# Kernel tuning notes

Hardware: AMD Instinct MI355X
Metric: run time of the kernel (lower is better)

Reference implementation:

```python
import jax, jax.numpy as jnp
from jax import lax
import numpy as np

B, N, P, NB = 64, 16, 20, 30      # frames, boxes/frame, num_persons, num_behaviors
C, F, OUT, SR = 1024, 14, 3, 2    # fmap channels, fmap size, roi output, sampling ratio
EPS = 1e-5


def roi_align_one(fmap, boxes):
    """fmap: [C,H,W]; boxes: [K,4]=(x1,y1,x2,y2) in fmap coords. Returns [K,C,OUT,OUT].
    torchvision-style roi_align (aligned=False) with fixed sampling_ratio=SR."""
    H, W = fmap.shape[1], fmap.shape[2]
    x1, y1, x2, y2 = boxes[:, 0], boxes[:, 1], boxes[:, 2], boxes[:, 3]
    rw = jnp.maximum(x2 - x1, 1.0)
    rh = jnp.maximum(y2 - y1, 1.0)
    S = OUT * SR
    pos = (jnp.arange(S, dtype=fmap.dtype) + 0.5) / SR            # sample pos in bin units
    ys = jnp.clip(y1[:, None] + pos[None, :] * (rh / OUT)[:, None], 0.0, H - 1.0)  # [K,S]
    xs = jnp.clip(x1[:, None] + pos[None, :] * (rw / OUT)[:, None], 0.0, W - 1.0)
    y0 = jnp.floor(ys); x0 = jnp.floor(xs)
    y0i = y0.astype(jnp.int32); x0i = x0.astype(jnp.int32)
    y1i = jnp.minimum(y0i + 1, H - 1); x1i = jnp.minimum(x0i + 1, W - 1)
    wy = ys - y0; wx = xs - x0                                     # [K,S]
    g = lambda yi, xi: fmap[:, yi[:, :, None], xi[:, None, :]]     # [C,K,S,S]
    v = (g(y0i, x0i) * ((1 - wy)[:, :, None] * (1 - wx)[:, None, :])
         + g(y0i, x1i) * ((1 - wy)[:, :, None] * wx[:, None, :])
         + g(y1i, x0i) * (wy[:, :, None] * (1 - wx)[:, None, :])
         + g(y1i, x1i) * (wy[:, :, None] * wx[:, None, :]))
    v = jnp.transpose(v, (1, 0, 2, 3))                             # [K,C,S,S]
    K = boxes.shape[0]
    return v.reshape(K, C, OUT, SR, OUT, SR).mean(axis=(3, 5))     # avg over samples


roi_align = jax.vmap(roi_align_one, in_axes=(0, 0))


def bn(x, g, b, m, v):
    s = (g / jnp.sqrt(v + EPS))[None, :, None, None]
    return x * s + (b - m * g / jnp.sqrt(v + EPS))[None, :, None, None]


def leaky(x):
    return jnp.where(x > 0, x, 0.1 * x)


def behavior_conv(x, w1, g1, b1, m1, v1, w2, g2, b2, m2, v2):
    dn = ('NCHW', 'OIHW', 'NCHW')
    x = lax.conv_general_dilated(x, w1, (1, 1), 'SAME', dimension_numbers=dn)
    x = leaky(bn(x, g1, b1, m1, v1))
    x = lax.conv_general_dilated(x, w2, (1, 1), 'SAME', dimension_numbers=dn)
    return leaky(bn(x, g2, b2, m2, v2))


def forward(fmap, boxes, conv1_w, bn1_g, bn1_b, bn1_m, bn1_v,
            conv2_w, bn2_g, bn2_b, bn2_m, bn2_v,
            conv1d_w, conv1d_b, fc1_w, fc1_b, fc2_w, fc2_b, person_idx):
    # --- global feature: ROI over the whole fmap per frame ---
    gbox = jnp.broadcast_to(jnp.array([[0.0, 0.0, F, F]], jnp.float32), (B, 1, 4))
    g_roi = roi_align(fmap, gbox).reshape(B, C, OUT, OUT)          # [B,1024,3,3]
    g_feat = behavior_conv(g_roi, conv1_w, bn1_g, bn1_b, bn1_m, bn1_v,
                           conv2_w, bn2_g, bn2_b, bn2_m, bn2_v)    # [B,256,3,3]
    g_feat = g_feat.reshape(B, 256 * OUT * OUT)                    # [B,2304]

    # --- per-box ROI features ---
    i_roi = roi_align(fmap, boxes).reshape(B * N, C, OUT, OUT)     # [B*N,1024,3,3]
    i_feat = behavior_conv(i_roi, conv1_w, bn1_g, bn1_b, bn1_m, bn1_v,
                           conv2_w, bn2_g, bn2_b, bn2_m, bn2_v)
    i_feat = i_feat.reshape(B, N, 256 * OUT * OUT)                 # [B,N,2304]

    # --- scatter-accumulate into behavior tensor [B,P,2304] ---
    behavior = jnp.broadcast_to(g_feat[:, None, :], (B, P, 2304))
    bidx = jnp.broadcast_to(jnp.arange(B)[:, None], (B, N))
    behavior = behavior.at[bidx, person_idx].add(i_feat)

    # --- temporal conv1d across the batch axis for every person slot ---
    x = jnp.transpose(behavior, (1, 2, 0))                         # [P,2304,B]
    x = lax.conv_general_dilated(x, conv1d_w, (1,), 'SAME',
                                 dimension_numbers=('NCH', 'OIH', 'NCH'))
    x = x + conv1d_b[None, :, None]                                # [P,2304,B]

    # --- gather each (frame, box)'s person feature at its frame and classify ---
    x = jnp.transpose(x, (2, 0, 1))                                # [B,P,2304]
    feats = jnp.take_along_axis(x, person_idx[:, :, None], axis=1) # [B,N,2304]
    h = jax.nn.relu(feats @ fc1_w + fc1_b)                         # dropout off (eval)
    return h @ fc2_w + fc2_b                                       # [B,N,NB]


def setup_inputs() -> dict:
    key = jax.random.key(0)
    ks = jax.random.split(key, 16)
    fmap = jax.random.normal(ks[0], (B, C, F, F), jnp.float32)
    lo = jax.random.uniform(ks[1], (B, N, 2), jnp.float32, 0.0, 9.0)
    sz = jax.random.uniform(ks[2], (B, N, 2), jnp.float32, 2.0, 5.0)
    hi = jnp.minimum(lo + sz, float(F))
    boxes = jnp.concatenate([lo, hi], axis=-1)                     # (x1,y1,x2,y2)
    person_idx = jax.random.randint(ks[3], (B, N), 0, P)
    s = lambda k, shape, fan: jax.random.normal(k, shape, jnp.float32) / np.sqrt(fan)
    return {
        'fmap': fmap, 'boxes': boxes, 'person_idx': person_idx,
        'conv1_w': s(ks[4], (512, 1024, 3, 3), 1024 * 9),
        'bn1_g': jnp.ones(512), 'bn1_b': jnp.zeros(512),
        'bn1_m': jnp.zeros(512), 'bn1_v': jnp.ones(512),
        'conv2_w': s(ks[5], (256, 512, 3, 3), 512 * 9),
        'bn2_g': jnp.ones(256), 'bn2_b': jnp.zeros(256),
        'bn2_m': jnp.zeros(256), 'bn2_v': jnp.ones(256),
        'conv1d_w': s(ks[6], (2304, 2304, 3), 2304 * 3),
        'conv1d_b': jnp.zeros(2304),
        'fc1_w': s(ks[7], (2304, 1024), 2304), 'fc1_b': jnp.zeros(1024),
        'fc2_w': s(ks[8], (1024, NB), 1024), 'fc2_b': jnp.zeros(NB),
    }


def reference(fmap, boxes, person_idx, conv1_w, bn1_g, bn1_b, bn1_m, bn1_v,
              conv2_w, bn2_g, bn2_b, bn2_m, bn2_v,
              conv1d_w, conv1d_b, fc1_w, fc1_b, fc2_w, fc2_b):
    return forward(fmap, boxes, conv1_w, bn1_g, bn1_b, bn1_m, bn1_v,
                   conv2_w, bn2_g, bn2_b, bn2_m, bn2_v,
                   conv1d_w, conv1d_b, fc1_w, fc1_b, fc2_w, fc2_b, person_idx)
```

## Files before the change

### kernel.cpp

```cpp
#include <hip/hip_runtime.h>
#include <hip/hip_bf16.h>
#include <cstdint>
#include <cstddef>

typedef __bf16 bf16;
typedef __bf16 bf16x8 __attribute__((ext_vector_type(8)));
typedef float f32x4 __attribute__((ext_vector_type(4)));

__device__ __forceinline__ void gload_lds16(const bf16* g, bf16* l) {
    __builtin_amdgcn_global_load_lds((const __attribute__((address_space(1))) void*)g,
                                     (__attribute__((address_space(3))) void*)l, 16, 0, 0);
}

__device__ __forceinline__ int block_tap_mask(int y) {
    int lo = (y * 128) / 1088;
    int hiRow = y * 128 + 127; if (hiRow > 9791) hiRow = 9791;
    int hi = hiRow / 1088;
    int msk = 0;
    for (int pos = lo; pos <= hi; ++pos) {
        int oy = pos / 3, ox = pos - oy * 3;
        int ym = oy == 0 ? 6 : (oy == 1 ? 7 : 3);
        int xm = ox == 0 ? 6 : (ox == 1 ? 7 : 3);
        #pragma unroll
        for (int ty = 0; ty < 3; ty++)
            #pragma unroll
            for (int tx = 0; tx < 3; tx++)
                if (((ym >> ty) & 1) & ((xm >> tx) & 1))
                    msk |= 1 << (ty * 3 + tx);
    }
    return msk;
}

template <int NT>
__global__ void __launch_bounds__(256) repack_w(const float* __restrict__ w, bf16* __restrict__ out,
                                                int OC, int IC) {
    int idx = blockIdx.x * 256 + threadIdx.x;
    if (idx >= OC * IC) return;
    int oc = idx / IC;
    int ic = idx - oc * IC;
    const float* src = w + (size_t)idx * NT;
    #pragma unroll
    for (int t = 0; t < NT; t++)
        out[(size_t)oc * NT * IC + t * IC + ic] = (bf16)src[t];
}

__global__ void __launch_bounds__(256) transpose_fc1(const float* __restrict__ w, bf16* __restrict__ out) {
    __shared__ float t[32][33];
    int iT = blockIdx.x * 32;
    int oT = blockIdx.y * 32;
    int tx = threadIdx.x, ty = threadIdx.y;
    #pragma unroll
    for (int j = 0; j < 4; j++)
        t[ty + j * 8][tx] = w[(size_t)(iT + ty + j * 8) * 1024 + oT + tx];
    __syncthreads();
    #pragma unroll
    for (int j = 0; j < 4; j++)
        out[(size_t)(oT + ty + j * 8) * 2304 + iT + tx] = (bf16)t[tx][ty + j * 8];
}

__global__ void __launch_bounds__(256) setup_all(int* __restrict__ rb1t, int* __restrict__ rb2t,
                                                 int* __restrict__ rb1dg, int* __restrict__ rbid,
                                                 int* __restrict__ tapmask,
                                                 int* __restrict__ tasks1, int* __restrict__ tasks2,
                                                 const int* __restrict__ pidx,
                                                 bf16* __restrict__ zp1, bf16* __restrict__ zp2,
                                                 bf16* __restrict__ zp3,
                                                 const float* g1, const float* b1, const float* m1, const float* v1,
                                                 const float* g2, const float* b2, const float* m2, const float* v2,
                                                 float* __restrict__ s1, float* __restrict__ t1,
                                                 float* __restrict__ s2, float* __restrict__ t2,
                                                 const float* __restrict__ fc2_w, bf16* __restrict__ w2t) {
    int m = blockIdx.x * 256 + threadIdx.x;
    if (m < 9 * 9856) {
        int tap = m / 9856, r = m - tap * 9856;
        int mm = r < 9792 ? r : 0;
        int pos = mm / 1088, img = mm - pos * 1088;
        int oy = pos / 3, ox = pos - oy * 3;
        int ty = tap / 3, tx = tap - ty * 3;
        int iy = oy + ty - 1, ix = ox + tx - 1;
        bool valid = (iy >= 0) & (iy < 3) & (ix >= 0) & (ix < 3);
        int cell = iy * 3 + ix;
        rb1t[m] = valid ? 1024 + (img * 9 + cell) * 1024 : 0;
        rb2t[m] = valid ? 512 + (cell * 1088 + img) * 512 : 0;
    }
    if (m < 77) tapmask[m] = block_tap_mask(m);
    if (blockIdx.x == 0) {
        __shared__ int sJ[77], sBase[78];
        __shared__ int ey[164], ej[164], ew[164];
        int t = threadIdx.x;
        if (t < 77) sJ[t] = (__popc(block_tap_mask(t)) + 2) / 3;
        __syncthreads();
        if (t == 0) {
            int acc = 0;
            for (int y = 0; y < 77; ++y) { sBase[y] = acc; acc += sJ[y]; }
            sBase[77] = acc;
        }
        __syncthreads();
        if (t < 77) {
            int T = __popc(block_tap_mask(t));
            int J = sJ[t];
            int w[3] = {0, 0, 0};
            for (int o = 0; o < T; ++o) w[o * J / T]++;
            for (int jj = 0; jj < J; ++jj) {
                int e = sBase[t] + jj;
                ey[e] = t; ej[e] = jj; ew[e] = w[jj];
            }
        }
        __syncthreads();
        if (t < 164) {
            int wv = ew[t], rank = 0;
            for (int e2 = 0; e2 < 164; ++e2)
                rank += (ew[e2] > wv) | ((ew[e2] == wv) & (e2 < t));
            int pk = (ey[t] << 5) | (ej[t] << 2);
            #pragma unroll
            for (int nt = 0; nt < 4; ++nt) tasks1[rank * 4 + nt] = pk | nt;
            #pragma unroll
            for (int nt = 0; nt < 2; ++nt) tasks2[rank * 2 + nt] = pk | nt;
        }
    }
    if (m < 3 * 1024) {
        int tap = m / 1024, r = m - tap * 1024;
        int b = r >> 4;
        int p = pidx[r];
        int tt = b + tap - 1;
        bool valid = (tt >= 0) & (tt < 64);
        rb1dg[m] = valid ? 2304 + (p * 64 + tt) * 2304 : 0;
    }
    if (m < 1024) rbid[m] = m * 2304;
    if (m < 30 * 1024) {
        int n = m / 1024, k = m - n * 1024;
        w2t[m] = (bf16)fc2_w[(size_t)k * 30 + n];
    }
    if (m < 1024) zp1[m] = (bf16)0.f;
    if (m < 512)  zp2[m] = (bf16)0.f;
    if (m < 2304) zp3[m] = (bf16)0.f;
    if (m < 512) {
        float sc = g1[m] * rsqrtf(v1[m] + 1e-5f);
        s1[m] = sc; t1[m] = b1[m] - m1[m] * sc;
    } else if (m < 768) {
        int i = m - 512;
        float sc = g2[i] * rsqrtf(v2[i] + 1e-5f);
        s2[i] = sc; t2[i] = b2[i] - m2[i] * sc;
    }
}

__global__ void __launch_bounds__(256) transpose_fmap(const float* __restrict__ fmap, bf16* __restrict__ fml) {
    __shared__ float t[32][33];
    int img = blockIdx.z;
    int hwT = blockIdx.x * 32;
    int cT  = blockIdx.y * 32;
    int tx = threadIdx.x, ty = threadIdx.y;
    #pragma unroll
    for (int j = 0; j < 4; j++) {
        int c = cT + ty + j * 8;
        int hw = hwT + tx;
        if (hw < 196)
            t[ty + j * 8][tx] = fmap[((size_t)img * 1024 + c) * 196 + hw];
    }
    __syncthreads();
    #pragma unroll
    for (int j = 0; j < 4; j++) {
        int hw = hwT + ty + j * 8;
        int c = cT + tx;
        if (hw < 196)
            fml[((size_t)img * 196 + hw) * 1024 + c] = (bf16)t[tx][ty + j * 8];
    }
}

__global__ void __launch_bounds__(128) roi_kernel2(const bf16* __restrict__ fml, const float* __restrict__ boxes,
                                                   bf16* __restrict__ a1c) {
    int box = blockIdx.x;
    int tid = threadIdx.x;
    float x1, y1, x2, y2;
    int img;
    if (box < 64) { img = box; x1 = 0.f; y1 = 0.f; x2 = 14.f; y2 = 14.f; }
    else {
        int ib = box - 64;
        img = ib >> 4;
        const float* bb = boxes + (size_t)ib * 4;
        x1 = bb[0]; y1 = bb[1]; x2 = bb[2]; y2 = bb[3];
    }
    float rw = fmaxf(x2 - x1, 1.f), rh = fmaxf(y2 - y1, 1.f);
    __shared__ float swy[6], swx[6];
    __shared__ int sy0[6], sx0[6];
    if (tid < 6) {
        int i = tid;
        float pos = ((float)i + 0.5f) * 0.5f;
        float yv = fminf(fmaxf(y1 + pos * (rh * (1.f / 3.f)), 0.f), 13.f);
        float y0 = floorf(yv);
        sy0[i] = (int)y0; swy[i] = yv - y0;
        float xv = fminf(fmaxf(x1 + pos * (rw * (1.f / 3.f)), 0.f), 13.f);
        float x0 = floorf(xv);
        sx0[i] = (int)x0; swx[i] = xv - x0;
    }
    __syncthreads();
    const bf16* base = fml + (size_t)img * 196 * 1024 + tid * 8;
    #pragma unroll
    for (int oy = 0; oy < 3; oy++) {
        #pragma unroll
        for (int ox = 0; ox < 3; ox++) {
            float acc[8];
            #pragma unroll
            for (int e = 0; e < 8; e++) acc[e] = 0.f;
            #pragma unroll
            for (int dy = 0; dy < 2; dy++) {
                int sy = 2 * oy + dy;
                int y0 = sy0[sy]; float wy = swy[sy];
                int y1i = min(y0 + 1, 13);
                #pragma unroll
                for (int dx = 0; dx < 2; dx++) {
                    int sx = 2 * ox + dx;
                    int x0 = sx0[sx]; float wx = swx[sx];
                    int x1i = min(x0 + 1, 13);
                    bf16x8 f00 = *(const bf16x8*)(base + (size_t)(y0 * 14 + x0) * 1024);
                    bf16x8 f01 = *(const bf16x8*)(base + (size_t)(y0 * 14 + x1i) * 1024);
                    bf16x8 f10 = *(const bf16x8*)(base + (size_t)(y1i * 14 + x0) * 1024);
                    bf16x8 f11 = *(const bf16x8*)(base + (size_t)(y1i * 14 + x1i) * 1024);
                    float w00 = (1.f - wy) * (1.f - wx), w01 = (1.f - wy) * wx;
                    float w10 = wy * (1.f - wx),         w11 = wy * wx;
                    #pragma unroll
                    for (int e = 0; e < 8; e++)
                        acc[e] += w00 * (float)f00[e] + w01 * (float)f01[e]
                                + w10 * (float)f10[e] + w11 * (float)f11[e];
                }
            }
            bf16x8 o;
            #pragma unroll
            for (int e = 0; e < 8; e++) o[e] = (bf16)(acc[e] * 0.25f);
            *(bf16x8*)(a1c + 1024 + ((size_t)box * 9 + oy * 3 + ox) * 1024 + tid * 8) = o;
        }
    }
}

__global__ void __launch_bounds__(256) assemble(const float* __restrict__ feat, const int* __restrict__ pidx,
                                                bf16* __restrict__ asm3) {
    int b = blockIdx.x;
    int p = blockIdx.y;
    __shared__ int idxs[16];
    if (threadIdx.x < 16) idxs[threadIdx.x] = pidx[b * 16 + threadIdx.x];
    __syncthreads();
    const float* g = feat + (size_t)b * 2304;
    for (int f = threadIdx.x; f < 2304; f += 256) {
        float v = g[f];
        #pragma unroll
        for (int n = 0; n < 16; n++)
            if (idxs[n] == p) v += feat[(size_t)(64 + b * 16 + n) * 2304 + f];
        asm3[2304 + ((size_t)p * 64 + b) * 2304 + f] = (bf16)v;
    }
}

template <int MODE, int NSPLIT>
__global__ void __launch_bounds__(256) gemm_k(const bf16* __restrict__ A, const int* __restrict__ rowtab,
                                              const bf16* __restrict__ Bw, float* __restrict__ outp,
                                              const int* __restrict__ tapmask,
                                              const int* __restrict__ tasklist) {
    constexpr int K   = MODE == 0 ? 9216 : MODE == 1 ? 4608 : MODE == 2 ? 6912 : 2304;
    constexpr int N   = MODE == 0 ? 512  : MODE == 1 ? 256  : MODE == 2 ? 2304 : 1024;
    constexpr int Cin = MODE == 0 ? 1024 : MODE == 1 ? 512  : 2304;
    constexpr int M   = MODE <= 1 ? 9792 : 1024;
    constexpr int MT  = MODE <= 1 ? 9856 : 1024;
    constexpr bool MPAD = (M % 128) != 0;
    constexpr int KTS = (K / 64) / NSPLIT;

    const int tid = threadIdx.x;
    const int lane = tid & 63, wave = tid >> 6;
    const int q = lane >> 4, ln16 = lane & 15;
    const int wr = wave >> 1, wc = wave & 1;

    __shared__ __align__(16) bf16 As[128 * 64];
    __shared__ __align__(16) bf16 Bs[128 * 64];

    const int sr = lane >> 3;
    const int sc = ((lane & 7) ^ sr) * 8;

    int bm, bn, z;
    int mask = 0, T = 0, J = 0, jsel = 0;
    if constexpr (MODE <= 1) {
        const int pk = tasklist[blockIdx.x];
        const int y = pk >> 5;
        jsel = (pk >> 2) & 7;
        const int nt = pk & 3;
        bm = y * 128; bn = nt * 128; z = jsel;
        mask = tapmask[y];
        T = __popc(mask);
        J = (T + 2) / 3;
    } else {
        bm = blockIdx.y * 128;
        bn = blockIdx.x * 128;
        z = blockIdx.z;
    }

    const bf16* gB[4];
    #pragma unroll
    for (int u = 0; u < 4; u++)
        gB[u] = Bw + (size_t)(bn + wave * 32 + u * 8 + sr) * K + sc;

    f32x4 acc[4][4];
    #pragma unroll
    for (int mt = 0; mt < 4; mt++)
        #pragma unroll
        for (int nn = 0; nn < 4; nn++)
            acc[mt][nn] = (f32x4){0.f, 0.f, 0.f, 0.f};

    if constexpr (MODE <= 1) {
        int ord = 0;
        for (int tap = 0; tap < 9; ++tap) {
            if (!((mask >> tap) & 1)) continue;
            const int o = ord++;
            if (o * J / T != jsel) continue;
            int rbA[4];
            #pragma unroll
            for (int u = 0; u < 4; u++)
                rbA[u] = rowtab[tap * MT + bm + wave * 32 + u * 8 + sr];
            for (int kk = 0; kk < Cin / 64; ++kk) {
                const int aoff = kk * 64 + sc;
                const int k0 = tap * Cin + kk * 64;

                __syncthreads();
                #pragma unroll
                for (int u = 0; u < 4; u++)
                    gload_lds16(A + (size_t)(rbA[u] + aoff), As + (wave * 32 + u * 8) * 64);
                #pragma unroll
                for (int u = 0; u < 4; u++)
                    gload_lds16(gB[u] + k0, Bs + (wave * 32 + u * 8) * 64);
                __syncthreads();

                #pragma unroll
                for (int s = 0; s < 2; s++) {
                    bf16x8 af[4], bfr[4];
                    #pragma unroll
                    for (int mt = 0; mt < 4; mt++) {
                        int r = wr * 64 + mt * 16 + ln16;
                        af[mt] = *(const bf16x8*)(As + r * 64 + (((4 * s + q) ^ (ln16 & 7)) << 3));
                    }
                    #pragma unroll
                    for (int nn = 0; nn < 4; nn++) {
                        int r = wc * 64 + nn * 16 + ln16;
                        bfr[nn] = *(const bf16x8*)(Bs + r * 64 + (((4 * s + q) ^ (ln16 & 7)) << 3));
                    }
                    #pragma unroll
                    for (int mt = 0; mt < 4; mt++)
                        #pragma unroll
                        for (int nn = 0; nn < 4; nn++)
                            acc[mt][nn] = __builtin_amdgcn_mfma_f32_16x16x32_bf16(af[mt], bfr[nn], acc[mt][nn], 0, 0, 0);
                }
            }
        }
    } else {
        int rbA[4];
        int curtap = -1;
        for (int kt = z * KTS; kt < z * KTS + KTS; kt++) {
            const int k0 = kt * 64;
            const int tap = k0 / Cin;
            const int inner = k0 - tap * Cin;
            if (tap != curtap) {
                curtap = tap;
                #pragma unroll
                for (int u = 0; u < 4; u++)
                    rbA[u] = rowtab[tap * MT + bm + wave * 32 + u * 8 + sr];
            }
            const int aoff = inner + sc;

            __syncthreads();
            #pragma unroll
            for (int u = 0; u < 4; u++)
                gload_lds16(A + (size_t)(rbA[u] + aoff), As + (wave * 32 + u * 8) * 64);
            #pragma unroll
            for (int u = 0; u < 4; u++)
                gload_lds16(gB[u] + k0, Bs + (wave * 32 + u * 8) * 64);
            __syncthreads();

            #pragma unroll
            for (int s = 0; s < 2; s++) {
                bf16x8 af[4], bfr[4];
                #pragma unroll
                for (int mt = 0; mt < 4; mt++) {
                    int r = wr * 64 + mt * 16 + ln16;
                    af[mt] = *(const bf16x8*)(As + r * 64 + (((4 * s + q) ^ (ln16 & 7)) << 3));
                }
                #pragma unroll
                for (int nn = 0; nn < 4; nn++) {
                    int r = wc * 64 + nn * 16 + ln16;
                    bfr[nn] = *(const bf16x8*)(Bs + r * 64 + (((4 * s + q) ^ (ln16 & 7)) << 3));
                }
                #pragma unroll
                for (int mt = 0; mt < 4; mt++)
                    #pragma unroll
                    for (int nn = 0; nn < 4; nn++)
                        acc[mt][nn] = __builtin_amdgcn_mfma_f32_16x16x32_bf16(af[mt], bfr[nn], acc[mt][nn], 0, 0, 0);
            }
        }
    }

    #pragma unroll
    for (int mt = 0; mt < 4; mt++) {
        int gmBase = bm + wr * 64 + mt * 16 + q * 4;
        #pragma unroll
        for (int r = 0; r < 4; r++) {
            int gm = gmBase + r;
            if (MPAD && gm >= M) continue;
            #pragma unroll
            for (int nn = 0; nn < 4; nn++) {
                int gn = bn + wc * 64 + nn * 16 + ln16;
                outp[((size_t)z * M + gm) * N + gn] = acc[mt][nn][r];
            }
        }
    }
}

__global__ void __launch_bounds__(256) reduce0_tiled(const float* __restrict__ part,
                                                     float* __restrict__ feat,
                                                     const float* __restrict__ s2, const float* __restrict__ t2,
                                                     const int* __restrict__ tapm) {
    int c = blockIdx.x;
    int t = threadIdx.x;
    float acc[9];
    #pragma unroll
    for (int r = 0; r < 9; r++) {
        int m = r * 1088 + c;
        int y = m >> 7;
        int J = (__popc(tapm[y]) + 2) / 3;
        const float* p0 = part + (size_t)m * 256 + t;
        float v = p0[0] + p0[(size_t)9792 * 256];
        if (J == 3) v += p0[(size_t)2 * 9792 * 256];
        acc[r] = v;
    }
    float s = s2[t], b = t2[t];
    __shared__ float L[9 * 257];
    #pragma unroll
    for (int r = 0; r < 9; r++) {
        float v = acc[r] * s + b;
        v = v > 0.f ? v : 0.1f * v;
        L[r * 257 + t] = v;
    }
    __syncthreads();
    float* fout = feat + (size_t)c * 2304;
    #pragma unroll
    for (int k = 0; k < 9; k++) {
        int f = t + k * 256;
        int oc = f / 9, pos = f - oc * 9;
        fout[f] = L[pos * 257 + oc];
    }
}

template <int RMODE>
__global__ void __launch_bounds__(256) reduce_k(const float* __restrict__ part, void* __restrict__ outp,
                                                const float* __restrict__ c0, const float* __restrict__ c1,
                                                const int* __restrict__ tapm) {
    constexpr int M = RMODE == 1 ? 1024 : RMODE == 2 ? 1024 : 9792;
    constexpr int N = RMODE == 1 ? 2304 : RMODE == 2 ? 1024 : 512;
    constexpr int S = RMODE == 1 ? 4    : RMODE == 2 ? 6    : 2;
    int idx = blockIdx.x * 256 + threadIdx.x;
    if (idx >= M * N) return;
    int m = idx / N, n = idx - m * N;
    float v = 0.f;
    #pragma unroll
    for (int s = 0; s < S; s++) v += part[(size_t)s * M * N + idx];
    if constexpr (RMODE == 1) {
        v += c0[n];
        ((bf16*)outp)[idx] = (bf16)v;
    } else if constexpr (RMODE == 2) {
        v = fmaxf(v + c0[n], 0.f);
        ((bf16*)outp)[idx] = (bf16)v;
    } else {
        int y = m >> 7;
        int J = (__popc(tapm[y]) + 2) / 3;
        if (J == 3) v += part[(size_t)2 * M * N + idx];
        v = v * c0[n] + c1[n];
        v = v > 0.f ? v : 0.1f * v;
        ((bf16*)outp)[512 + (size_t)m * 512 + n] = (bf16)v;
    }
}

__global__ void __launch_bounds__(256) fc2_kernel(const bf16* __restrict__ h, const bf16* __restrict__ w2t,
                                                  const float* __restrict__ b2, float* __restrict__ out) {
    int tid = threadIdx.x;
    int m = blockIdx.x * 8 + (tid >> 5);
    int n = tid & 31;
    int n2 = n < 30 ? n : 29;
    const bf16* hr = h + (size_t)m * 1024;
    const bf16* wr = w2t + (size_t)n2 * 1024;
    float acc = 0.f;
    for (int k = 0; k < 1024; k += 8) {
        bf16x8 hv = *(const bf16x8*)(hr + k);
        bf16x8 wv = *(const bf16x8*)(wr + k);
        #pragma unroll
        for (int e = 0; e < 8; e++) acc += (float)hv[e] * (float)wv[e];
    }
    if (n < 30) out[(size_t)m * 30 + n] = acc + b2[n];
}

extern "C" void kernel_launch(void* const* d_in, const int* in_sizes, int n_in,
                              void* d_out, int out_size, void* d_ws, size_t ws_size,
                              hipStream_t stream) {
    const float* fmap     = (const float*)d_in[0];
    const float* boxes    = (const float*)d_in[1];
    const int*   pidx     = (const int*)d_in[2];
    const float* conv1_w  = (const float*)d_in[3];
    const float* bn1_g    = (const float*)d_in[4];
    const float* bn1_b    = (const float*)d_in[5];
    const float* bn1_m    = (const float*)d_in[6];
    const float* bn1_v    = (const float*)d_in[7];
    const float* conv2_w  = (const float*)d_in[8];
    const float* bn2_g    = (const float*)d_in[9];
    const float* bn2_b    = (const float*)d_in[10];
    const float* bn2_m    = (const float*)d_in[11];
    const float* bn2_v    = (const float*)d_in[12];
    const float* conv1d_w = (const float*)d_in[13];
    const float* conv1d_b = (const float*)d_in[14];
    const float* fc1_w    = (const float*)d_in[15];
    const float* fc1_b    = (const float*)d_in[16];
    const float* fc2_w    = (const float*)d_in[17];
    const float* fc2_b    = (const float*)d_in[18];
    float* out = (float*)d_out;

    char* ws = (char*)d_ws;

    float* s1    = (float*)(ws + 0);
    float* t1    = (float*)(ws + 2048);
    float* s2    = (float*)(ws + 4096);
    float* t2    = (float*)(ws + 5120);
    int*   rbid  = (int*)(ws + 6144);
    int*   rb1dg = (int*)(ws + 10240);
    int*   tapm  = (int*)(ws + 22528);
    int*   rb1t  = (int*)(ws + 25600);
    int*   rb2t  = (int*)(ws + 380416);
    int*   tasks1 = (int*)(ws + 735232);
    int*   tasks2 = (int*)(ws + 738944);
    bf16*  fml    = (bf16*)(ws + 768000);
    float* part1  = (float*)(ws + 768000);
    float* part2  = (float*)(ws + 768000);
    float* part1d = (float*)(ws + 768000);
    float* partfc = (float*)(ws + 768000);
    bf16*  a1c    = (bf16*)(ws + 60930048);
    bf16*  wb1d   = (bf16*)(ws + 60930048);
    bf16*  fc1t   = (bf16*)(ws + 92780544);
    bf16*  xbuf   = (bf16*)(ws + 97499136);
    bf16*  hbuf   = (bf16*)(ws + 102217728);
    bf16*  w2t    = (bf16*)(ws + 104314880);
    bf16*  wb1    = (bf16*)(ws + 104857600);
    bf16*  wb2    = (bf16*)(ws + 114294784);
    bf16*  a2c    = (bf16*)(ws + 116654080);
    bf16*  asm3   = (bf16*)(ws + 126682112);
    float* feat   = (float*)(ws + 132584960);

    bf16* zp1 = a1c;
    bf16* zp2 = a2c;
    bf16* zp3 = asm3;

    setup_all<<<(9 * 9856 + 255) / 256, 256, 0, stream>>>(rb1t, rb2t, rb1dg, rbid, tapm,
                                                          tasks1, tasks2, pidx,
                                                          zp1, zp2, zp3,
                                                          bn1_g, bn1_b, bn1_m, bn1_v,
                                                          bn2_g, bn2_b, bn2_m, bn2_v,
                                                          s1, t1, s2, t2, fc2_w, w2t);
    repack_w<9><<<(512 * 1024 + 255) / 256, 256, 0, stream>>>(conv1_w, wb1, 512, 1024);
    repack_w<9><<<(256 * 512 + 255) / 256, 256, 0, stream>>>(conv2_w, wb2, 256, 512);

    transpose_fmap<<<dim3(7, 32, 64), dim3(32, 8), 0, stream>>>(fmap, fml);
    roi_kernel2<<<1088, 128, 0, stream>>>(fml, boxes, a1c);

    gemm_k<0, 3><<<656, 256, 0, stream>>>(a1c, rb1t, wb1, part1, tapm, tasks1);
    reduce_k<3><<<(9792 * 512 + 255) / 256, 256, 0, stream>>>(part1, a2c, s1, t1, tapm);

    repack_w<3><<<(2304 * 2304 + 255) / 256, 256, 0, stream>>>(conv1d_w, wb1d, 2304, 2304);
    transpose_fc1<<<dim3(72, 32), dim3(32, 8), 0, stream>>>(fc1_w, fc1t);

    gemm_k<1, 3><<<328, 256, 0, stream>>>(a2c, rb2t, wb2, part2, tapm, tasks2);
    reduce0_tiled<<<1088, 256, 0, stream>>>(part2, feat, s2, t2, tapm);
    assemble<<<dim3(64, 20), 256, 0, stream>>>(feat, pidx, asm3);
    gemm_k<2, 4><<<dim3(18, 8, 4), 256, 0, stream>>>(asm3, rb1dg, wb1d, part1d, tapm, nullptr);
    reduce_k<1><<<(1024 * 2304 + 255) / 256, 256, 0, stream>>>(part1d, xbuf, conv1d_b, nullptr, nullptr);
    gemm_k<3, 6><<<dim3(8, 8, 6), 256, 0, stream>>>(xbuf, rbid, fc1t, partfc, tapm, nullptr);
    reduce_k<2><<<(1024 * 1024 + 255) / 256, 256, 0, stream>>>(partfc, hbuf, fc1_b, nullptr, nullptr);
    fc2_kernel<<<128, 256, 0, stream>>>(hbuf, w2t, fc2_b, out);
    (void)in_sizes; (void)n_in; (void)out_size; (void)ws_size;
}
```

Before: 456.5 us.

## Retune split-K factors, reorder task lists per XCD, fuse conv weight repacks

Lowers the split-K factor for the conv2 task GEMM (taps split into groups of up to four), the conv1d GEMM and the fc1 GEMM, cutting partial-sum traffic and reduction work. The setup kernel builds separate task lists for conv1 and conv2 and interleaves task indices in groups of eight, likely to spread heavy tasks across chiplets. The two 3x3 weight repack kernels merge into one launch. Fewer splits mean fewer blocks and longer per-block K loops, which may reduce occupancy.

New measurement: 465.0 us. About the same (+1.9%).

```diff
diff --git a/kernel.cpp b/kernel.cpp
--- a/kernel.cpp
+++ b/kernel.cpp
@@ -42,6 +42,27 @@
     #pragma unroll
     for (int t = 0; t < NT; t++)
         out[(size_t)oc * NT * IC + t * IC + ic] = (bf16)src[t];
+}
+
+__global__ void __launch_bounds__(256) repack_w9_both(const float* __restrict__ wa, bf16* __restrict__ oa,
+                                                      const float* __restrict__ wb, bf16* __restrict__ ob) {
+    int idx = blockIdx.x * 256 + threadIdx.x;
+    if (idx < 512 * 1024) {
+        int oc = idx >> 10, ic = idx & 1023;
+        const float* src = wa + (size_t)idx * 9;
+        #pragma unroll
+        for (int t = 0; t < 9; t++)
+            oa[(size_t)oc * 9216 + t * 1024 + ic] = (bf16)src[t];
+    } else {
+        int k = idx - 512 * 1024;
+        if (k < 256 * 512) {
+            int oc = k >> 9, ic = k & 511;
+            const float* src = wb + (size_t)k * 9;
+            #pragma unroll
+            for (int t = 0; t < 9; t++)
+                ob[(size_t)oc * 4608 + t * 512 + ic] = (bf16)src[t];
+        }
+    }
 }
 
 __global__ void __launch_bounds__(256) transpose_fc1(const float* __restrict__ w, bf16* __restrict__ out) {
@@ -85,37 +106,60 @@
     }
     if (m < 77) tapmask[m] = block_tap_mask(m);
     if (blockIdx.x == 0) {
-        __shared__ int sJ[77], sBase[78];
-        __shared__ int ey[164], ej[164], ew[164];
+        __shared__ int sT[77], sB1[78], sB2[78];
+        __shared__ int e1y[164], e1j[164], e1w[164];
+        __shared__ int e2y[130], e2j[130], e2w[130];
         int t = threadIdx.x;
-        if (t < 77) sJ[t] = (__popc(block_tap_mask(t)) + 2) / 3;
+        if (t < 77) sT[t] = __popc(block_tap_mask(t));
         __syncthreads();
         if (t == 0) {
-            int acc = 0;
-            for (int y = 0; y < 77; ++y) { sBase[y] = acc; acc += sJ[y]; }
-            sBase[77] = acc;
+            int a1 = 0, a2 = 0;
+            for (int y = 0; y < 77; ++y) {
+                sB1[y] = a1; a1 += (sT[y] + 2) / 3;
+                sB2[y] = a2; a2 += (sT[y] + 3) / 4;
+            }
+            sB1[77] = a1;
+            sB2[77] = a2;
         }
         __syncthreads();
         if (t < 77) {
-            int T = __popc(block_tap_mask(t));
-            int J = sJ[t];
-            int w[3] = {0, 0, 0};
-            for (int o = 0; o < T; ++o) w[o * J / T]++;
-            for (int jj = 0; jj < J; ++jj) {
-                int e = sBase[t] + jj;
-                ey[e] = t; ej[e] = jj; ew[e] = w[jj];
+            int T = sT[t];
+            int J1 = (T + 2) / 3, J2 = (T + 3) / 4;
+            int w1[3] = {0, 0, 0}, w2[3] = {0, 0, 0};
+            for (int o = 0; o < T; ++o) { w1[o * J1 / T]++; w2[o * J2 / T]++; }
+            for (int jj = 0; jj < J1; ++jj) {
+                int e = sB1[t] + jj;
+                e1y[e] = t; e1j[e] = jj; e1w[e] = w1[jj];
+            }
+            for (int jj = 0; jj < J2; ++jj) {
+                int e = sB2[t] + jj;
+                e2y[e] = t; e2j[e] = jj; e2w[e] = w2[jj];
             }
         }
         __syncthreads();
         if (t < 164) {
-            int wv = ew[t], rank = 0;
-            for (int e2 = 0; e2 < 164; ++e2)
-                rank += (ew[e2] > wv) | ((ew[e2] == wv) & (e2 < t));
-            int pk = (ey[t] << 5) | (ej[t] << 2);
-            #pragma unroll
-            for (int nt = 0; nt < 4; ++nt) tasks1[rank * 4 + nt] = pk | nt;
-            #pragma unroll
-            for (int nt = 0; nt < 2; ++nt) tasks2[rank * 2 + nt] = pk | nt;
+            int wv = e1w[t], rank = 0;
+            for (int e2i = 0; e2i < 164; ++e2i)
+                rank += (e1w[e2i] > wv) | ((e1w[e2i] == wv) & (e2i < t));
+            int pk = (e1y[t] << 5) | (e1j[t] << 2);
+            #pragma unroll
+            for (int nt = 0; nt < 4; ++nt) {
+                int idx = (rank < 160) ? ((rank & 7) + (((rank >> 3) * 4 + nt) << 3))
+                                       : (640 + (rank - 160) * 4 + nt);
+                tasks1[idx] = pk | nt;
+            }
+        }
+        if (t < 130) {
+            int wv = e2w[t], rank = 0;
+            for (int e2i = 0; e2i < 130; ++e2i)
+                rank += (e2w[e2i] > wv) | ((e2w[e2i] == wv) & (e2i < t));
+            int pk = (e2y[t] << 5) | (e2j[t] << 2);
+            #pragma unroll
+            for (int nt = 0; nt < 2; ++nt) {
+                int idx = (rank < 128) ? ((rank & 7) + (((rank >> 3) * 2 + nt) << 3))
+                                       : (256 + (rank - 128) * 2 + nt);
+                tasks2[idx] = pk | nt;
+            }
         }
     }
     if (m < 3 * 1024) {
@@ -283,7 +327,7 @@
         bm = y * 128; bn = nt * 128; z = jsel;
         mask = tapmask[y];
         T = __popc(mask);
-        J = (T + 2) / 3;
+        J = MODE == 0 ? (T + 2) / 3 : (T + 3) / 4;
     } else {
         bm = blockIdx.y * 128;
         bn = blockIdx.x * 128;
@@ -419,10 +463,11 @@
     for (int r = 0; r < 9; r++) {
         int m = r * 1088 + c;
         int y = m >> 7;
-        int J = (__popc(tapm[y]) + 2) / 3;
+        int J = (__popc(tapm[y]) + 3) / 4;
         const float* p0 = part + (size_t)m * 256 + t;
-        float v = p0[0] + p0[(size_t)9792 * 256];
-        if (J == 3) v += p0[(size_t)2 * 9792 * 256];
+        float v = p0[0];
+        if (J >= 2) v += p0[(size_t)9792 * 256];
+        if (J >= 3) v += p0[(size_t)2 * 9792 * 256];
         acc[r] = v;
     }
     float s = s2[t], b = t2[t];
@@ -449,7 +494,7 @@
                                                 const int* __restrict__ tapm) {
     constexpr int M = RMODE == 1 ? 1024 : RMODE == 2 ? 1024 : 9792;
     constexpr int N = RMODE == 1 ? 2304 : RMODE == 2 ? 1024 : 512;
-    constexpr int S = RMODE == 1 ? 4    : RMODE == 2 ? 6    : 2;
+    constexpr int S = RMODE == 1 ? 3    : RMODE == 2 ? 4    : 2;
     int idx = blockIdx.x * 256 + threadIdx.x;
     if (idx >= M * N) return;
     int m = idx / N, n = idx - m * N;
@@ -554,8 +599,7 @@
                                                           bn1_g, bn1_b, bn1_m, bn1_v,
                                                           bn2_g, bn2_b, bn2_m, bn2_v,
                                                           s1, t1, s2, t2, fc2_w, w2t);
-    repack_w<9><<<(512 * 1024 + 255) / 256, 256, 0, stream>>>(conv1_w, wb1, 512, 1024);
-    repack_w<9><<<(256 * 512 + 255) / 256, 256, 0, stream>>>(conv2_w, wb2, 256, 512);
+    repack_w9_both<<<2560, 256, 0, stream>>>(conv1_w, wb1, conv2_w, wb2);
 
     transpose_fmap<<<dim3(7, 32, 64), dim3(32, 8), 0, stream>>>(fmap, fml);
     roi_kernel2<<<1088, 128, 0, stream>>>(fml, boxes, a1c);
@@ -566,12 +610,12 @@
     repack_w<3><<<(2304 * 2304 + 255) / 256, 256, 0, stream>>>(conv1d_w, wb1d, 2304, 2304);
     transpose_fc1<<<dim3(72, 32), dim3(32, 8), 0, stream>>>(fc1_w, fc1t);
 
-    gemm_k<1, 3><<<328, 256, 0, stream>>>(a2c, rb2t, wb2, part2, tapm, tasks2);
+    gemm_k<1, 3><<<260, 256, 0, stream>>>(a2c, rb2t, wb2, part2, tapm, tasks2);
     reduce0_tiled<<<1088, 256, 0, stream>>>(part2, feat, s2, t2, tapm);
     assemble<<<dim3(64, 20), 256, 0, stream>>>(feat, pidx, asm3);
-    gemm_k<2, 4><<<dim3(18, 8, 4), 256, 0, stream>>>(asm3, rb1dg, wb1d, part1d, tapm, nullptr);
+    gemm_k<2, 3><<<dim3(18, 8, 3), 256, 0, stream>>>(asm3, rb1dg, wb1d, part1d, tapm, nullptr);
     reduce_k<1><<<(1024 * 2304 + 255) / 256, 256, 0, stream>>>(part1d, xbuf, conv1d_b, nullptr, nullptr);
-    gemm_k<3, 6><<<dim3(8, 8, 6), 256, 0, stream>>>(xbuf, rbid, fc1t, partfc, tapm, nullptr);
+    gemm_k<3, 4><<<dim3(8, 8, 4), 256, 0, stream>>>(xbuf, rbid, fc1t, partfc, tapm, nullptr);
     reduce_k<2><<<(1024 * 1024 + 255) / 256, 256, 0, stream>>>(partfc, hbuf, fc1_b, nullptr, nullptr);
     fc2_kernel<<<128, 256, 0, stream>>>(hbuf, w2t, fc2_b, out);
     (void)in_sizes; (void)n_in; (void)out_size; (void)ws_size;
```
